# Performance work log

Measured on AMD Instinct MI355X. Metric: run time of the kernel, lower is better.

Reference implementation:

```python
import jax, jax.numpy as jnp
import numpy as np

DIM = 2048
N_HEADS = 16
KV_LORA = 512
NOPE = 128
ROPE = 64
V_DIM = 128
QK_DIM = NOPE + ROPE  # 192
B, S = 2, 2048
ROPE_THETA = 10000.0
ROPE_FACTOR = 40.0
BETA_FAST, BETA_SLOW = 32, 1
ORIG_LEN, MAX_LEN = 4096, 16384
MSCALE_ARG = 1.0
EPS = 1e-6


def _precompute_freqs(seqlen):
    # DeepSeek YaRN-corrected rotary frequencies (interleaved-pair convention).
    d = ROPE
    freqs = 1.0 / (ROPE_THETA ** (np.arange(0, d, 2, dtype=np.float64) / d))
    if MAX_LEN > ORIG_LEN:
        def corr_dim(n_rot):
            return d * np.log(ORIG_LEN / (n_rot * 2 * np.pi)) / (2 * np.log(ROPE_THETA))
        low = max(int(np.floor(corr_dim(BETA_FAST))), 0)
        high = min(int(np.ceil(corr_dim(BETA_SLOW))), d - 1)
        smooth = 1.0 - np.clip((np.arange(d // 2) - low) / max(high - low, 1e-3), 0, 1)
        freqs = freqs / ROPE_FACTOR * (1 - smooth) + freqs * smooth
    t = np.arange(seqlen, dtype=np.float64)
    ang = np.outer(t, freqs)  # [S, d/2]
    return np.cos(ang).astype(np.float32), np.sin(ang).astype(np.float32)


def softmax_scale():
    scale = QK_DIM ** -0.5
    if MAX_LEN > ORIG_LEN:
        m = 0.1 * MSCALE_ARG * float(np.log(ROPE_FACTOR)) + 1.0
        scale = scale * m * m
    return scale


def setup_inputs() -> dict:
    key = jax.random.key(0)
    ks = jax.random.split(key, 6)
    w_std = 0.02
    fc, fs = _precompute_freqs(S)
    return {
        "x": jax.random.normal(ks[0], (B, S, DIM), jnp.float32),
        "wq": jax.random.normal(ks[1], (N_HEADS * QK_DIM, DIM), jnp.float32) * w_std,
        "wkv_a": jax.random.normal(ks[2], (KV_LORA + ROPE, DIM), jnp.float32) * w_std,
        "kv_norm_w": jnp.ones((KV_LORA,), jnp.float32),
        "wkv_b": jax.random.normal(ks[3], (N_HEADS * (NOPE + V_DIM), KV_LORA), jnp.float32) * w_std,
        "wo": jax.random.normal(ks[4], (DIM, N_HEADS * V_DIM), jnp.float32) * w_std,
        "freqs_cos": jnp.asarray(fc),
        "freqs_sin": jnp.asarray(fs),
    }


def _apply_rotary(x, cos, sin):
    # x: [B, S, H, d]; interleaved complex pairs, cos/sin: [S, d/2]
    xr = x.reshape(*x.shape[:-1], -1, 2)
    x_re, x_im = xr[..., 0], xr[..., 1]
    c = cos[None, :, None, :]
    s = sin[None, :, None, :]
    y_re = x_re * c - x_im * s
    y_im = x_re * s + x_im * c
    return jnp.stack((y_re, y_im), axis=-1).reshape(x.shape)


def _rmsnorm(x, w):
    return x * jax.lax.rsqrt(jnp.mean(x * x, axis=-1, keepdims=True) + EPS) * w


def reference(x, wq, wkv_a, kv_norm_w, wkv_b, wo, freqs_cos, freqs_sin):
    b, s, _ = x.shape
    # Q projection (q_lora_rank == 0 path)
    q = (x @ wq.T).reshape(b, s, N_HEADS, QK_DIM)
    q_nope, q_pe = q[..., :NOPE], q[..., NOPE:]
    q_pe = _apply_rotary(q_pe, freqs_cos, freqs_sin)
    # Low-rank KV compression
    kv = x @ wkv_a.T  # [B, S, 512+64]
    kv_c, k_pe = kv[..., :KV_LORA], kv[..., KV_LORA:]
    k_pe = _apply_rotary(k_pe[:, :, None, :], freqs_cos, freqs_sin)  # [B,S,1,64]
    kv_c = _rmsnorm(kv_c, kv_norm_w)
    kvb = (kv_c @ wkv_b.T).reshape(b, s, N_HEADS, NOPE + V_DIM)
    k_nope, v = kvb[..., :NOPE], kvb[..., NOPE:]
    k = jnp.concatenate([k_nope, jnp.broadcast_to(k_pe, (b, s, N_HEADS, ROPE))], axis=-1)
    # Causal attention
    scores = jnp.einsum("bshd,bthd->bhst", q, k) * softmax_scale()
    causal = jnp.tril(jnp.ones((s, s), bool))
    scores = jnp.where(causal[None, None], scores, jnp.float32(-1e30))
    p = jax.nn.softmax(scores, axis=-1)
    out = jnp.einsum("bhst,bthd->bshd", p, v).reshape(b, s, N_HEADS * V_DIM)
    return out @ wo.T
```

## Files before the change

### kernel.cpp

```cpp
#include <hip/hip_runtime.h>
#include <math.h>

#define NH      16
#define D_NOPE  128
#define D_ROPE  64
#define D_QK    192
#define D_V     128
#define KV_LORA 512
#define NB      2
#define SEQ     2048
#define NTOK    (NB*SEQ)
#define QROW    (NH*D_QK)
#define KVBROW  (NH*(D_NOPE+D_V))
#define EPSF    1e-6f

typedef unsigned short u16;
typedef float  floatx4 __attribute__((ext_vector_type(4)));
typedef __bf16 bf16x8  __attribute__((ext_vector_type(8)));
typedef u16    u16x4   __attribute__((ext_vector_type(4)));
typedef u16    u16x8   __attribute__((ext_vector_type(8)));

__device__ __forceinline__ u16 f2bf(float f) {
    unsigned u = __builtin_bit_cast(unsigned, f);
    return (u16)((u + 0x7fffu + ((u >> 16) & 1u)) >> 16);
}

__device__ __forceinline__ void async_copy16(const void* g, void* l) {
    __builtin_amdgcn_global_load_lds(
        (const __attribute__((address_space(1))) unsigned int*)g,
        (__attribute__((address_space(3))) unsigned int*)l,
        16, 0, 0);
}

__global__ __launch_bounds__(256) void cast_all(const float* __restrict__ x,
                                                const float* __restrict__ wq,
                                                const float* __restrict__ wkva,
                                                const float* __restrict__ wkvb,
                                                const float* __restrict__ wo,
                                                u16* __restrict__ xb,
                                                u16* __restrict__ wqb,
                                                u16* __restrict__ wkvab,
                                                u16* __restrict__ wkvbb,
                                                u16* __restrict__ wob) {
    int blk = blockIdx.x;
    const float* src; u16* dst; bool pad = false;
    if (blk < 8192)        { src = x;    dst = xb; }
    else if (blk < 14336)  { blk -= 8192;  src = wq;   dst = wqb; }
    else if (blk < 15616)  { blk -= 14336; src = wkva; dst = wkvab; pad = true; }
    else if (blk < 17664)  { blk -= 15616; src = wkvb; dst = wkvbb; }
    else                   { blk -= 17664; src = wo;   dst = wob; }
    const int i = (blk * 256 + threadIdx.x) * 4;
    u16x4 o;
    if (pad && (i >> 11) >= 576) {
        o[0] = 0; o[1] = 0; o[2] = 0; o[3] = 0;
    } else {
        const float4 v = *(const float4*)&src[i];
        o[0] = f2bf(v.x); o[1] = f2bf(v.y); o[2] = f2bf(v.z); o[3] = f2bf(v.w);
    }
    *(u16x4*)&dst[i] = o;
}

template<int MODE>
__global__ __launch_bounds__(256) void gemm_mfma(const u16* __restrict__ A,
                                                 const u16* __restrict__ B,
                                                 void* __restrict__ Cout,
                                                 u16* __restrict__ kbuf,
                                                 u16* __restrict__ vT,
                                                 int M, int N, int K) {
    __shared__ u16 As[128 * 32];
    __shared__ u16 Bs[128 * 32];
    const int tid  = threadIdx.x;
    const int wave = tid >> 6, lane = tid & 63;
    const int m0 = blockIdx.y * 128, n0 = blockIdx.x * 128;
    const int wm = (wave & 1) * 64, wn = (wave >> 1) * 64;

    const int srow = wave * 32 + (lane >> 2);
    const int kch  = (lane & 3) * 8;
    const u16* gA0 = A + (size_t)(m0 + srow) * K + kch;
    const u16* gA1 = gA0 + (size_t)16 * K;
    const u16* gB0 = B + (size_t)(n0 + srow) * K + kch;
    const u16* gB1 = gB0 + (size_t)16 * K;
    u16* lA0 = &As[(wave * 32) * 32];
    u16* lA1 = &As[(wave * 32 + 16) * 32];
    u16* lB0 = &Bs[(wave * 32) * 32];
    u16* lB1 = &Bs[(wave * 32 + 16) * 32];

    floatx4 acc[4][4];
#pragma unroll
    for (int i = 0; i < 4; ++i)
#pragma unroll
        for (int j = 0; j < 4; ++j) acc[i][j] = 0.f;

    const int lrow = lane & 15;
    const int lkh  = (lane >> 4) * 8;

    for (int k0 = 0; k0 < K; k0 += 32) {
        __syncthreads();
        async_copy16(gA0 + k0, lA0);
        async_copy16(gA1 + k0, lA1);
        async_copy16(gB0 + k0, lB0);
        async_copy16(gB1 + k0, lB1);
        __syncthreads();
        bf16x8 a[4], b[4];
#pragma unroll
        for (int mi = 0; mi < 4; ++mi)
            a[mi] = *(const bf16x8*)&As[(wm + mi * 16 + lrow) * 32 + lkh];
#pragma unroll
        for (int ni = 0; ni < 4; ++ni)
            b[ni] = *(const bf16x8*)&Bs[(wn + ni * 16 + lrow) * 32 + lkh];
#pragma unroll
        for (int mi = 0; mi < 4; ++mi)
#pragma unroll
            for (int ni = 0; ni < 4; ++ni)
                acc[mi][ni] = __builtin_amdgcn_mfma_f32_16x16x32_bf16(
                    a[mi], b[ni], acc[mi][ni], 0, 0, 0);
    }

    const int crow = (lane >> 4) * 4, ccol = lane & 15;
#pragma unroll
    for (int mi = 0; mi < 4; ++mi)
#pragma unroll
        for (int ni = 0; ni < 4; ++ni) {
            const int m = m0 + wm + mi * 16 + crow;
            const int c = n0 + wn + ni * 16 + ccol;
            if (MODE == 0) {
                float* cp = (float*)Cout + (size_t)m * N + c;
#pragma unroll
                for (int r = 0; r < 4; ++r) cp[(size_t)r * N] = acc[mi][ni][r];
            } else if (MODE == 1) {
                u16* cp = (u16*)Cout + (size_t)m * N + c;
#pragma unroll
                for (int r = 0; r < 4; ++r) cp[(size_t)r * N] = f2bf(acc[mi][ni][r]);
            } else {
                const int hh = c >> 8, j = c & 255;
                const int bb = m >> 11, t = m & 2047;
                if (j < 128) {
#pragma unroll
                    for (int r = 0; r < 4; ++r)
                        kbuf[(((size_t)hh * 2 + bb) * 2048 + t + r) * 192 + j] =
                            f2bf(acc[mi][ni][r]);
                } else {
                    u16x4 pk;
#pragma unroll
                    for (int r = 0; r < 4; ++r) pk[r] = f2bf(acc[mi][ni][r]);
                    *(u16x4*)&vT[(((size_t)hh * 2 + bb) * 128 + (j - 128)) * 2048 + t] = pk;
                }
            }
        }
}


__global__ __launch_bounds__(256) void kv_fix(const float* __restrict__ kv_raw,
                                              const float* __restrict__ w,
                                              const float* __restrict__ fcos,
                                              const float* __restrict__ fsin,
                                              u16* __restrict__ kvn_bf,
                                              u16* __restrict__ kbuf) {
    const int row = blockIdx.x;
    const int tid = threadIdx.x;
    const float* src = kv_raw + (size_t)row * 640;
    const float v0 = src[tid];
    const float v1 = src[256 + tid];
    float ss = v0 * v0 + v1 * v1;
#pragma unroll
    for (int off = 32; off > 0; off >>= 1) ss += __shfl_down(ss, off, 64);
    __shared__ float red[4];
    __shared__ float kpe_s[64];
    if ((tid & 63) == 0) red[tid >> 6] = ss;
    if (tid < 32) {
        const int s = row & (SEQ - 1);
        const float c  = fcos[s * 32 + tid];
        const float sn = fsin[s * 32 + tid];
        const float xr = src[KV_LORA + 2 * tid];
        const float xi = src[KV_LORA + 2 * tid + 1];
        kpe_s[2 * tid]     = xr * c - xi * sn;
        kpe_s[2 * tid + 1] = xr * sn + xi * c;
    }
    __syncthreads();
    const float tot = red[0] + red[1] + red[2] + red[3];
    const float inv = rsqrtf(tot * (1.0f / KV_LORA) + EPSF);
    kvn_bf[(size_t)row * KV_LORA + tid]       = f2bf(v0 * inv * w[tid]);
    kvn_bf[(size_t)row * KV_LORA + 256 + tid] = f2bf(v1 * inv * w[256 + tid]);
    const int bb = row >> 11, t = row & 2047;
    const int hh = tid >> 4, dg = (tid & 15) * 4;
    u16x4 pk;
#pragma unroll
    for (int j = 0; j < 4; ++j) pk[j] = f2bf(kpe_s[dg + j]);
    *(u16x4*)&kbuf[(((size_t)hh * 2 + bb) * 2048 + t) * 192 + 128 + dg] = pk;
}

__global__ __launch_bounds__(256, 2) void attn_mfma(const u16* __restrict__ qbf,
                                                    const u16* __restrict__ kbuf,
                                                    const u16* __restrict__ vT,
                                                    u16* __restrict__ att,
                                                    float scale) {
    __shared__ __attribute__((aligned(16))) u16 Ks[2][6 * 64 * 32];
    __shared__ __attribute__((aligned(16))) u16 Vs[2 * 128 * 32];
    __shared__ __attribute__((aligned(16))) u16 Ps[4][16 * 72];
    const int x = blockIdx.x;
    const int qt_base = (x & 1) ? (15 - (x >> 1)) : (x >> 1);
    const int qt = blockIdx.z ? (15 - qt_base) : qt_base;
    const int h = blockIdx.y, b = blockIdx.z;
    const int tid = threadIdx.x, wave = tid >> 6, lane = tid & 63;
    const int l15 = lane & 15, lg = lane >> 4;
    const int lgs = lg ^ ((l15 >> 1) & 3);

    const u16* kb_base = kbuf + ((size_t)(h * 2 + b)) * 2048 * 192;
    const u16* vt_base = vT   + ((size_t)(h * 2 + b)) * 128 * 2048;

    int qrow[2];
    bf16x8 qf[2][6];
#pragma unroll
    for (int g = 0; g < 2; ++g) {
        qrow[g] = qt * 128 + g * 64 + wave * 16 + l15;
        const size_t qoff = ((size_t)(b * SEQ + qrow[g])) * QROW + h * 192 + lg * 8;
#pragma unroll
        for (int s = 0; s < 6; ++s) qf[g][s] = *(const bf16x8*)&qbf[qoff + s * 32];
    }

    floatx4 oacc[2][8];
#pragma unroll
    for (int g = 0; g < 2; ++g)
#pragma unroll
        for (int v = 0; v < 8; ++v) oacc[g][v] = 0.f;
    float m_run[2] = {-1e30f, -1e30f}, l_run[2] = {0.f, 0.f};

    auto stageK = [&](int bufi, int tt) {
#pragma unroll
        for (int i = 0; i < 6; ++i) {
            const int base = (wave * 6 + i) * 64;
            const int slot = base + lane;
            const int s = slot >> 8, r = slot & 255, tk = r >> 2, ch = r & 3;
            const int chs = ch ^ ((tk >> 1) & 3);
            async_copy16(kb_base + ((size_t)(tt + tk)) * 192 + s * 32 + chs * 8,
                         &Ks[bufi][base * 8]);
        }
    };
    auto stageV = [&](int tt) {
#pragma unroll
        for (int i = 0; i < 4; ++i) {
            const int base = (wave * 4 + i) * 64;
            const int slot = base + lane;
            const int s = slot >> 9, r = slot & 511, v = r >> 2, ch = r & 3;
            const int chs = ch ^ ((v >> 1) & 3);
            async_copy16(vt_base + ((size_t)v) * 2048 + tt + s * 32 + chs * 8,
                         &Vs[base * 8]);
        }
    };

    const int kt_max = 2 * qt + 1;
    stageK(0, 0);

    for (int kt = 0; kt <= kt_max; ++kt) {
        const int t0 = kt * 64;
        const int cur = kt & 1;

        stageV(t0);
        if (kt < kt_max) {
            stageK(cur ^ 1, t0 + 64);
            asm volatile("s_waitcnt vmcnt(10)" ::: "memory");
        } else {
            asm volatile("s_waitcnt vmcnt(4)" ::: "memory");
        }
        __builtin_amdgcn_s_barrier();

        floatx4 sacc[2][4];
#pragma unroll
        for (int g = 0; g < 2; ++g)
#pragma unroll
            for (int mt = 0; mt < 4; ++mt) sacc[g][mt] = 0.f;
        __builtin_amdgcn_s_setprio(1);
#pragma unroll
        for (int s = 0; s < 6; ++s) {
#pragma unroll
            for (int mt = 0; mt < 4; ++mt) {
                const bf16x8 kf = *(const bf16x8*)&Ks[cur][(s * 64 + mt * 16 + l15) * 32 + lgs * 8];
#pragma unroll
                for (int g = 0; g < 2; ++g)
                    sacc[g][mt] = __builtin_amdgcn_mfma_f32_16x16x32_bf16(
                        kf, qf[g][s], sacc[g][mt], 0, 0, 0);
            }
        }
        __builtin_amdgcn_s_setprio(0);

        u16x4 pk[2][4];
#pragma unroll
        for (int g = 0; g < 2; ++g) {
            const bool full = (t0 + 63) <= (qt * 128 + g * 64 + wave * 16);
            float p[16];
            float tmax = -1e30f;
#pragma unroll
            for (int mt = 0; mt < 4; ++mt)
#pragma unroll
                for (int r = 0; r < 4; ++r) {
                    float v = sacc[g][mt][r] * scale;
                    if (!full) {
                        const int tglob = t0 + mt * 16 + lg * 4 + r;
                        v = (tglob <= qrow[g]) ? v : -1e30f;
                    }
                    p[mt * 4 + r] = v;
                    tmax = fmaxf(tmax, v);
                }
            tmax = fmaxf(tmax, __shfl_xor(tmax, 16));
            tmax = fmaxf(tmax, __shfl_xor(tmax, 32));
            const bool defer = __all(tmax <= m_run[g] + 8.0f);
            float alph = 1.0f;
            float mnew = m_run[g];
            if (!defer) {
                mnew = fmaxf(m_run[g], tmax);
                alph = __expf(m_run[g] - mnew);
                m_run[g] = mnew;
            }
            float rsum = 0.f;
#pragma unroll
            for (int k = 0; k < 16; ++k) { p[k] = __expf(p[k] - mnew); rsum += p[k]; }
            rsum += __shfl_xor(rsum, 16);
            rsum += __shfl_xor(rsum, 32);
            if (!defer) {
                l_run[g] = l_run[g] * alph + rsum;
                float af[4];
#pragma unroll
                for (int r = 0; r < 4; ++r) af[r] = __shfl(alph, lg * 4 + r);
#pragma unroll
                for (int vt = 0; vt < 8; ++vt)
#pragma unroll
                    for (int r = 0; r < 4; ++r) oacc[g][vt][r] *= af[r];
            } else {
                l_run[g] += rsum;
            }
#pragma unroll
            for (int mt = 0; mt < 4; ++mt)
#pragma unroll
                for (int r = 0; r < 4; ++r) pk[g][mt][r] = f2bf(p[mt * 4 + r]);
        }

        bf16x8 pf[2][2];
#pragma unroll
        for (int g = 0; g < 2; ++g) {
#pragma unroll
            for (int mt = 0; mt < 4; ++mt)
                *(u16x4*)&Ps[wave][l15 * 72 + mt * 16 + lg * 4] = pk[g][mt];
#pragma unroll
            for (int s = 0; s < 2; ++s)
                pf[g][s] = *(const bf16x8*)&Ps[wave][l15 * 72 + s * 32 + lg * 8];
        }

        if (kt < kt_max) asm volatile("s_waitcnt vmcnt(6)" ::: "memory");
        else             asm volatile("s_waitcnt vmcnt(0)" ::: "memory");
        __builtin_amdgcn_s_barrier();

        __builtin_amdgcn_s_setprio(1);
#pragma unroll
        for (int s = 0; s < 2; ++s)
#pragma unroll
            for (int vt = 0; vt < 8; ++vt) {
                const bf16x8 vf = *(const bf16x8*)&Vs[(s * 128 + vt * 16 + l15) * 32 + lgs * 8];
                oacc[0][vt] = __builtin_amdgcn_mfma_f32_16x16x32_bf16(
                    pf[0][s], vf, oacc[0][vt], 0, 0, 0);
                oacc[1][vt] = __builtin_amdgcn_mfma_f32_16x16x32_bf16(
                    pf[1][s], vf, oacc[1][vt], 0, 0, 0);
            }
        __builtin_amdgcn_s_setprio(0);

        __builtin_amdgcn_s_barrier();
    }
#pragma unroll
    for (int g = 0; g < 2; ++g) {
        float lf[4];
#pragma unroll
        for (int r = 0; r < 4; ++r) lf[r] = 1.0f / __shfl(l_run[g], lg * 4 + r);
#pragma unroll
        for (int vt = 0; vt < 8; ++vt)
#pragma unroll
            for (int r = 0; r < 4; ++r) {
                const int orow = b * SEQ + qt * 128 + g * 64 + wave * 16 + lg * 4 + r;
                att[(size_t)orow * 2048 + h * 128 + vt * 16 + l15] =
                    f2bf(oacc[g][vt][r] * lf[r]);
            }
    }
}

extern "C" void kernel_launch(void* const* d_in, const int* in_sizes, int n_in,
                              void* d_out, int out_size, void* d_ws, size_t ws_size,
                              hipStream_t stream) {
    const float* x     = (const float*)d_in[0];
    const float* wq    = (const float*)d_in[1];
    const float* wkv_a = (const float*)d_in[2];
    const float* knw   = (const float*)d_in[3];
    const float* wkv_b = (const float*)d_in[4];
    const float* wo    = (const float*)d_in[5];
    const float* fcos  = (const float*)d_in[6];
    const float* fsin  = (const float*)d_in[7];
    float* out = (float*)d_out;

    char* w = (char*)d_ws;
    u16*   x_bf    = (u16*)w;  w += (size_t)NTOK * 2048 * 2;
    u16*   wq_bf   = (u16*)w;  w += (size_t)QROW * 2048 * 2;
    u16*   wkva_bf = (u16*)w;  w += (size_t)640 * 2048 * 2;
    u16*   wkvb_bf = (u16*)w;  w += (size_t)KVBROW * KV_LORA * 2;
    u16*   wo_bf   = (u16*)w;  w += (size_t)2048 * 2048 * 2;
    u16*   q_bf    = (u16*)w;  w += (size_t)NTOK * QROW * 2;
    float* kv_raw  = (float*)w; w += (size_t)NTOK * 640 * 4;
    u16*   kvn_bf  = (u16*)w;  w += (size_t)NTOK * KV_LORA * 2;
    u16*   kbuf    = (u16*)w;  w += (size_t)NH * NB * SEQ * 192 * 2;
    u16*   vT      = (u16*)w;  w += (size_t)NH * NB * 128 * SEQ * 2;
    u16*   att_bf  = (u16*)w;  w += (size_t)NTOK * 2048 * 2;

    const double mm = 0.1 * 1.0 * log(40.0) + 1.0;
    const float scale = (float)((1.0 / sqrt((double)D_QK)) * mm * mm);

    dim3 blk(256);
    cast_all<<<dim3(21760), blk, 0, stream>>>(x, wq, wkv_a, wkv_b, wo,
                                              x_bf, wq_bf, wkva_bf, wkvb_bf, wo_bf);
    gemm_mfma<1><<<dim3(QROW / 128, NTOK / 128), blk, 0, stream>>>(
        x_bf, wq_bf, q_bf, nullptr, nullptr, NTOK, QROW, 2048);
    gemm_mfma<0><<<dim3(640 / 128, NTOK / 128), blk, 0, stream>>>(
        x_bf, wkva_bf, kv_raw, nullptr, nullptr, NTOK, 640, 2048);
    kv_fix<<<dim3(NTOK), blk, 0, stream>>>(kv_raw, knw, fcos, fsin, kvn_bf, kbuf);
    gemm_mfma<2><<<dim3(KVBROW / 128, NTOK / 128), blk, 0, stream>>>(
        kvn_bf, wkvb_bf, nullptr, kbuf, vT, NTOK, KVBROW, KV_LORA);
    attn_mfma<<<dim3(SEQ / 128, NH, NB), blk, 0, stream>>>(q_bf, kbuf, vT, att_bf, scale);
    gemm_mfma<0><<<dim3(2048 / 128, NTOK / 128), blk, 0, stream>>>(
        att_bf, wo_bf, out, nullptr, nullptr, NTOK, 2048, 2048);
}
```

Baseline: 432.4 us.

## Balance causal attention work by pairing short and long query chunks per wave

Result: slower. 488.7 us (+13.0%).

```diff
diff --git a/kernel.cpp b/kernel.cpp
--- a/kernel.cpp
+++ b/kernel.cpp
@@ -197,25 +197,51 @@
     __shared__ __attribute__((aligned(16))) u16 Ks[2][6 * 64 * 32];
     __shared__ __attribute__((aligned(16))) u16 Vs[2 * 128 * 32];
     __shared__ __attribute__((aligned(16))) u16 Ps[4][16 * 72];
-    const int x = blockIdx.x;
-    const int qt_base = (x & 1) ? (15 - (x >> 1)) : (x >> 1);
-    const int qt = blockIdx.z ? (15 - qt_base) : qt_base;
+    const int j = blockIdx.x;
     const int h = blockIdx.y, b = blockIdx.z;
     const int tid = threadIdx.x, wave = tid >> 6, lane = tid & 63;
     const int l15 = lane & 15, lg = lane >> 4;
     const int lgs = lg ^ ((l15 >> 1) & 3);
 
+    const int c0 = j + 16 * wave;
+    const int c1 = j + 16 * (7 - wave);
+    const int ktmax0 = c0 >> 2;
+    const int ktmax1 = c1 >> 2;
+    const int KT = 28 + (j >> 2);
+
     const u16* kb_base = kbuf + ((size_t)(h * 2 + b)) * 2048 * 192;
     const u16* vt_base = vT   + ((size_t)(h * 2 + b)) * 128 * 2048;
 
-    int qrow[2];
+    const int qmin[2] = {16 * c0, 16 * c1};
+    const int qrow[2] = {16 * c0 + l15, 16 * c1 + l15};
     bf16x8 qf[2][6];
 #pragma unroll
     for (int g = 0; g < 2; ++g) {
-        qrow[g] = qt * 128 + g * 64 + wave * 16 + l15;
         const size_t qoff = ((size_t)(b * SEQ + qrow[g])) * QROW + h * 192 + lg * 8;
 #pragma unroll
         for (int s = 0; s < 6; ++s) qf[g][s] = *(const bf16x8*)&qbf[qoff + s * 32];
+    }
+
+    const u16* ksrc[6]; u16* kdstA[6]; u16* kdstB[6];
+#pragma unroll
+    for (int i = 0; i < 6; ++i) {
+        const int base = (wave * 6 + i) * 64;
+        const int slot = base + lane;
+        const int s = slot >> 8, r = slot & 255, tk = r >> 2, ch = r & 3;
+        const int chs = ch ^ ((tk >> 1) & 3);
+        ksrc[i]  = kb_base + (size_t)tk * 192 + s * 32 + chs * 8;
+        kdstA[i] = &Ks[0][base * 8];
+        kdstB[i] = &Ks[1][base * 8];
+    }
+    const u16* vsrc[4]; u16* vdst[4];
+#pragma unroll
+    for (int i = 0; i < 4; ++i) {
+        const int base = (wave * 4 + i) * 64;
+        const int slot = base + lane;
+        const int s = slot >> 9, r = slot & 511, v = r >> 2, ch = r & 3;
+        const int chs = ch ^ ((v >> 1) & 3);
+        vsrc[i] = vt_base + (size_t)v * 2048 + s * 32 + chs * 8;
+        vdst[i] = &Vs[base * 8];
     }
 
     floatx4 oacc[2][8];
@@ -225,39 +251,21 @@
         for (int v = 0; v < 8; ++v) oacc[g][v] = 0.f;
     float m_run[2] = {-1e30f, -1e30f}, l_run[2] = {0.f, 0.f};
 
-    auto stageK = [&](int bufi, int tt) {
-#pragma unroll
-        for (int i = 0; i < 6; ++i) {
-            const int base = (wave * 6 + i) * 64;
-            const int slot = base + lane;
-            const int s = slot >> 8, r = slot & 255, tk = r >> 2, ch = r & 3;
-            const int chs = ch ^ ((tk >> 1) & 3);
-            async_copy16(kb_base + ((size_t)(tt + tk)) * 192 + s * 32 + chs * 8,
-                         &Ks[bufi][base * 8]);
-        }
-    };
-    auto stageV = [&](int tt) {
-#pragma unroll
-        for (int i = 0; i < 4; ++i) {
-            const int base = (wave * 4 + i) * 64;
-            const int slot = base + lane;
-            const int s = slot >> 9, r = slot & 511, v = r >> 2, ch = r & 3;
-            const int chs = ch ^ ((v >> 1) & 3);
-            async_copy16(vt_base + ((size_t)v) * 2048 + tt + s * 32 + chs * 8,
-                         &Vs[base * 8]);
-        }
-    };
-
-    const int kt_max = 2 * qt + 1;
-    stageK(0, 0);
-
-    for (int kt = 0; kt <= kt_max; ++kt) {
+#pragma unroll
+    for (int i = 0; i < 6; ++i) async_copy16(ksrc[i], kdstA[i]);
+
+    for (int kt = 0; kt <= KT; ++kt) {
         const int t0 = kt * 64;
         const int cur = kt & 1;
-
-        stageV(t0);
-        if (kt < kt_max) {
-            stageK(cur ^ 1, t0 + 64);
+        const bool act0 = (kt <= ktmax0), act1 = (kt <= ktmax1);
+
+#pragma unroll
+        for (int i = 0; i < 4; ++i) async_copy16(vsrc[i] + t0, vdst[i]);
+        if (kt < KT) {
+            const size_t koff = (size_t)(t0 + 64) * 192;
+            u16* const* kd = cur ? kdstA : kdstB;
+#pragma unroll
+            for (int i = 0; i < 6; ++i) async_copy16(ksrc[i] + koff, kd[i]);
             asm volatile("s_waitcnt vmcnt(10)" ::: "memory");
         } else {
             asm volatile("s_waitcnt vmcnt(4)" ::: "memory");
@@ -269,24 +277,37 @@
         for (int g = 0; g < 2; ++g)
 #pragma unroll
             for (int mt = 0; mt < 4; ++mt) sacc[g][mt] = 0.f;
-        __builtin_amdgcn_s_setprio(1);
-#pragma unroll
-        for (int s = 0; s < 6; ++s) {
-#pragma unroll
-            for (int mt = 0; mt < 4; ++mt) {
-                const bf16x8 kf = *(const bf16x8*)&Ks[cur][(s * 64 + mt * 16 + l15) * 32 + lgs * 8];
-#pragma unroll
-                for (int g = 0; g < 2; ++g)
-                    sacc[g][mt] = __builtin_amdgcn_mfma_f32_16x16x32_bf16(
-                        kf, qf[g][s], sacc[g][mt], 0, 0, 0);
-            }
-        }
-        __builtin_amdgcn_s_setprio(0);
+        if (act1) {
+            __builtin_amdgcn_s_setprio(1);
+            if (act0) {
+#pragma unroll
+                for (int s = 0; s < 6; ++s)
+#pragma unroll
+                    for (int mt = 0; mt < 4; ++mt) {
+                        const bf16x8 kf = *(const bf16x8*)&Ks[cur][(s * 64 + mt * 16 + l15) * 32 + lgs * 8];
+                        sacc[0][mt] = __builtin_amdgcn_mfma_f32_16x16x32_bf16(
+                            kf, qf[0][s], sacc[0][mt], 0, 0, 0);
+                        sacc[1][mt] = __builtin_amdgcn_mfma_f32_16x16x32_bf16(
+                            kf, qf[1][s], sacc[1][mt], 0, 0, 0);
+                    }
+            } else {
+#pragma unroll
+                for (int s = 0; s < 6; ++s)
+#pragma unroll
+                    for (int mt = 0; mt < 4; ++mt) {
+                        const bf16x8 kf = *(const bf16x8*)&Ks[cur][(s * 64 + mt * 16 + l15) * 32 + lgs * 8];
+                        sacc[1][mt] = __builtin_amdgcn_mfma_f32_16x16x32_bf16(
+                            kf, qf[1][s], sacc[1][mt], 0, 0, 0);
+                    }
+            }
+            __builtin_amdgcn_s_setprio(0);
+        }
 
         u16x4 pk[2][4];
 #pragma unroll
         for (int g = 0; g < 2; ++g) {
-            const bool full = (t0 + 63) <= (qt * 128 + g * 64 + wave * 16);
+            if (!(g ? act1 : act0)) continue;
+            const bool full = (t0 + 63) <= qmin[g];
             float p[16];
             float tmax = -1e30f;
 #pragma unroll
@@ -337,6 +358,7 @@
         bf16x8 pf[2][2];
 #pragma unroll
         for (int g = 0; g < 2; ++g) {
+            if (!(g ? act1 : act0)) continue;
 #pragma unroll
             for (int mt = 0; mt < 4; ++mt)
                 *(u16x4*)&Ps[wave][l15 * 72 + mt * 16 + lg * 4] = pk[g][mt];
@@ -345,22 +367,35 @@
                 pf[g][s] = *(const bf16x8*)&Ps[wave][l15 * 72 + s * 32 + lg * 8];
         }
 
-        if (kt < kt_max) asm volatile("s_waitcnt vmcnt(6)" ::: "memory");
-        else             asm volatile("s_waitcnt vmcnt(0)" ::: "memory");
+        if (kt < KT) asm volatile("s_waitcnt vmcnt(6)" ::: "memory");
+        else         asm volatile("s_waitcnt vmcnt(0)" ::: "memory");
         __builtin_amdgcn_s_barrier();
 
-        __builtin_amdgcn_s_setprio(1);
-#pragma unroll
-        for (int s = 0; s < 2; ++s)
-#pragma unroll
-            for (int vt = 0; vt < 8; ++vt) {
-                const bf16x8 vf = *(const bf16x8*)&Vs[(s * 128 + vt * 16 + l15) * 32 + lgs * 8];
-                oacc[0][vt] = __builtin_amdgcn_mfma_f32_16x16x32_bf16(
-                    pf[0][s], vf, oacc[0][vt], 0, 0, 0);
-                oacc[1][vt] = __builtin_amdgcn_mfma_f32_16x16x32_bf16(
-                    pf[1][s], vf, oacc[1][vt], 0, 0, 0);
-            }
-        __builtin_amdgcn_s_setprio(0);
+        if (act1) {
+            __builtin_amdgcn_s_setprio(1);
+            if (act0) {
+#pragma unroll
+                for (int s = 0; s < 2; ++s)
+#pragma unroll
+                    for (int vt = 0; vt < 8; ++vt) {
+                        const bf16x8 vf = *(const bf16x8*)&Vs[(s * 128 + vt * 16 + l15) * 32 + lgs * 8];
+                        oacc[0][vt] = __builtin_amdgcn_mfma_f32_16x16x32_bf16(
+                            pf[0][s], vf, oacc[0][vt], 0, 0, 0);
+                        oacc[1][vt] = __builtin_amdgcn_mfma_f32_16x16x32_bf16(
+                            pf[1][s], vf, oacc[1][vt], 0, 0, 0);
+                    }
+            } else {
+#pragma unroll
+                for (int s = 0; s < 2; ++s)
+#pragma unroll
+                    for (int vt = 0; vt < 8; ++vt) {
+                        const bf16x8 vf = *(const bf16x8*)&Vs[(s * 128 + vt * 16 + l15) * 32 + lgs * 8];
+                        oacc[1][vt] = __builtin_amdgcn_mfma_f32_16x16x32_bf16(
+                            pf[1][s], vf, oacc[1][vt], 0, 0, 0);
+                    }
+            }
+            __builtin_amdgcn_s_setprio(0);
+        }
 
         __builtin_amdgcn_s_barrier();
     }
@@ -373,7 +408,7 @@
         for (int vt = 0; vt < 8; ++vt)
 #pragma unroll
             for (int r = 0; r < 4; ++r) {
-                const int orow = b * SEQ + qt * 128 + g * 64 + wave * 16 + lg * 4 + r;
+                const int orow = b * SEQ + qmin[g] + lg * 4 + r;
                 att[(size_t)orow * 2048 + h * 128 + vt * 16 + l15] =
                     f2bf(oacc[g][vt][r] * lf[r]);
             }
@@ -419,7 +454,7 @@
     kv_fix<<<dim3(NTOK), blk, 0, stream>>>(kv_raw, knw, fcos, fsin, kvn_bf, kbuf);
     gemm_mfma<2><<<dim3(KVBROW / 128, NTOK / 128), blk, 0, stream>>>(
         kvn_bf, wkvb_bf, nullptr, kbuf, vT, NTOK, KVBROW, KV_LORA);
-    attn_mfma<<<dim3(SEQ / 128, NH, NB), blk, 0, stream>>>(q_bf, kbuf, vT, att_bf, scale);
+    attn_mfma<<<dim3(16, NH, NB), blk, 0, stream>>>(q_bf, kbuf, vT, att_bf, scale);
     gemm_mfma<0><<<dim3(2048 / 128, NTOK / 128), blk, 0, stream>>>(
         att_bf, wo_bf, out, nullptr, nullptr, NTOK, 2048, 2048);
 }
```

## Pair complementary causal q-tiles per 8-wave block with shared double-buffered K/V

Applied to the files above, without the earlier changes.

New measurement: 468.0 us. 8.2% more time.

```diff
diff --git a/kernel.cpp b/kernel.cpp
--- a/kernel.cpp
+++ b/kernel.cpp
@@ -189,18 +189,20 @@
     *(u16x4*)&kbuf[(((size_t)hh * 2 + bb) * 2048 + t) * 192 + 128 + dg] = pk;
 }
 
-__global__ __launch_bounds__(256, 2) void attn_mfma(const u16* __restrict__ qbf,
+#define KS_HALF (6 * 64 * 32)
+#define VS_HALF (2 * 128 * 32)
+__global__ __launch_bounds__(512, 2) void attn_mfma(const u16* __restrict__ qbf,
                                                     const u16* __restrict__ kbuf,
                                                     const u16* __restrict__ vT,
                                                     u16* __restrict__ att,
                                                     float scale) {
-    __shared__ __attribute__((aligned(16))) u16 Ks[2][6 * 64 * 32];
-    __shared__ __attribute__((aligned(16))) u16 Vs[2 * 128 * 32];
-    __shared__ __attribute__((aligned(16))) u16 Ps[4][16 * 72];
-    const int x = blockIdx.x;
-    const int qt_base = (x & 1) ? (15 - (x >> 1)) : (x >> 1);
-    const int qt = blockIdx.z ? (15 - qt_base) : qt_base;
-    const int h = blockIdx.y, b = blockIdx.z;
+    __shared__ __attribute__((aligned(16))) u16 KsF[2 * KS_HALF];
+    __shared__ __attribute__((aligned(16))) u16 VsF[2 * VS_HALF];
+    __shared__ __attribute__((aligned(16))) u16 Ps[8][16 * 72];
+    const int hb = blockIdx.x;
+    const int qa = blockIdx.y;
+    const int qb = 15 - qa;
+    const int h = hb >> 1, b = hb & 1;
     const int tid = threadIdx.x, wave = tid >> 6, lane = tid & 63;
     const int l15 = lane & 15, lg = lane >> 4;
     const int lgs = lg ^ ((l15 >> 1) & 3);
@@ -208,14 +210,41 @@
     const u16* kb_base = kbuf + ((size_t)(h * 2 + b)) * 2048 * 192;
     const u16* vt_base = vT   + ((size_t)(h * 2 + b)) * 128 * 2048;
 
-    int qrow[2];
+    const int qbase0 = qa * 128 + wave * 16;
+    const int qbase1 = qb * 128 + wave * 16;
     bf16x8 qf[2][6];
-#pragma unroll
-    for (int g = 0; g < 2; ++g) {
-        qrow[g] = qt * 128 + g * 64 + wave * 16 + l15;
-        const size_t qoff = ((size_t)(b * SEQ + qrow[g])) * QROW + h * 192 + lg * 8;
-#pragma unroll
-        for (int s = 0; s < 6; ++s) qf[g][s] = *(const bf16x8*)&qbf[qoff + s * 32];
+    {
+        const size_t q0 = ((size_t)(b * SEQ + qbase0 + l15)) * QROW + h * 192 + lg * 8;
+        const size_t q1 = ((size_t)(b * SEQ + qbase1 + l15)) * QROW + h * 192 + lg * 8;
+#pragma unroll
+        for (int s = 0; s < 6; ++s) {
+            qf[0][s] = *(const bf16x8*)&qbf[q0 + s * 32];
+            qf[1][s] = *(const bf16x8*)&qbf[q1 + s * 32];
+        }
+    }
+
+    const u16* ksrc0; const u16* ksrc1; const u16* ksrc2;
+    int kbo0, kbo1, kbo2;
+    {
+        const int b0 = (wave * 3 + 0) * 64, s0 = (b0 + lane) >> 8, r0 = (b0 + lane) & 255;
+        const int b1 = (wave * 3 + 1) * 64, s1 = (b1 + lane) >> 8, r1 = (b1 + lane) & 255;
+        const int b2 = (wave * 3 + 2) * 64, s2 = (b2 + lane) >> 8, r2 = (b2 + lane) & 255;
+        const int tk0 = r0 >> 2, tk1 = r1 >> 2, tk2 = r2 >> 2;
+        ksrc0 = kb_base + (size_t)tk0 * 192 + s0 * 32 + ((r0 & 3) ^ ((tk0 >> 1) & 3)) * 8;
+        ksrc1 = kb_base + (size_t)tk1 * 192 + s1 * 32 + ((r1 & 3) ^ ((tk1 >> 1) & 3)) * 8;
+        ksrc2 = kb_base + (size_t)tk2 * 192 + s2 * 32 + ((r2 & 3) ^ ((tk2 >> 1) & 3)) * 8;
+        kbo0 = b0 * 8; kbo1 = b1 * 8; kbo2 = b2 * 8;
+    }
+    const u16* vsrc0; const u16* vsrc1;
+    int vbo0, vbo1;
+    {
+        const int b0 = (wave * 2 + 0) * 64, s0 = (b0 + lane) >> 9, r0 = (b0 + lane) & 511;
+        const int b1 = (wave * 2 + 1) * 64, s1 = (b1 + lane) >> 9, r1 = (b1 + lane) & 511;
+        const int v0 = r0 >> 2, v1 = r1 >> 2;
+        vsrc0 = vt_base + (size_t)v0 * 2048 + s0 * 32 + ((r0 & 3) ^ ((v0 >> 1) & 3)) * 8;
+        vsrc1 = vt_base + (size_t)v1 * 2048 + s1 * 32 + ((v1 >> 1 & 3) != 0 ? ((r1 & 3) ^ ((v1 >> 1) & 3)) : (r1 & 3)) * 8;
+        vsrc1 = vt_base + (size_t)v1 * 2048 + s1 * 32 + ((r1 & 3) ^ ((v1 >> 1) & 3)) * 8;
+        vbo0 = b0 * 8; vbo1 = b1 * 8;
     }
 
     floatx4 oacc[2][8];
@@ -225,78 +254,80 @@
         for (int v = 0; v < 8; ++v) oacc[g][v] = 0.f;
     float m_run[2] = {-1e30f, -1e30f}, l_run[2] = {0.f, 0.f};
 
-    auto stageK = [&](int bufi, int tt) {
-#pragma unroll
-        for (int i = 0; i < 6; ++i) {
-            const int base = (wave * 6 + i) * 64;
-            const int slot = base + lane;
-            const int s = slot >> 8, r = slot & 255, tk = r >> 2, ch = r & 3;
-            const int chs = ch ^ ((tk >> 1) & 3);
-            async_copy16(kb_base + ((size_t)(tt + tk)) * 192 + s * 32 + chs * 8,
-                         &Ks[bufi][base * 8]);
-        }
-    };
-    auto stageV = [&](int tt) {
-#pragma unroll
-        for (int i = 0; i < 4; ++i) {
-            const int base = (wave * 4 + i) * 64;
-            const int slot = base + lane;
-            const int s = slot >> 9, r = slot & 511, v = r >> 2, ch = r & 3;
-            const int chs = ch ^ ((v >> 1) & 3);
-            async_copy16(vt_base + ((size_t)v) * 2048 + tt + s * 32 + chs * 8,
-                         &Vs[base * 8]);
-        }
-    };
-
-    const int kt_max = 2 * qt + 1;
-    stageK(0, 0);
-
-    for (int kt = 0; kt <= kt_max; ++kt) {
+    const int nt = 32 - 2 * qa;
+    const int ktmax0 = 2 * qa + 1;
+
+    async_copy16(ksrc0, &KsF[kbo0]);
+    async_copy16(ksrc1, &KsF[kbo1]);
+    async_copy16(ksrc2, &KsF[kbo2]);
+    async_copy16(vsrc0, &VsF[vbo0]);
+    async_copy16(vsrc1, &VsF[vbo1]);
+
+    for (int kt = 0; kt < nt; ++kt) {
         const int t0 = kt * 64;
         const int cur = kt & 1;
-
-        stageV(t0);
-        if (kt < kt_max) {
-            stageK(cur ^ 1, t0 + 64);
-            asm volatile("s_waitcnt vmcnt(10)" ::: "memory");
+        const int kco = cur * KS_HALF;
+        const int vco = cur * VS_HALF;
+        const bool act0 = (kt <= ktmax0);
+
+        asm volatile("s_waitcnt vmcnt(0)" ::: "memory");
+        __builtin_amdgcn_s_barrier();
+
+        if (kt + 1 < nt) {
+            const int kno = (cur ^ 1) * KS_HALF;
+            const int vno = (cur ^ 1) * VS_HALF;
+            const size_t ko = (size_t)(t0 + 64) * 192;
+            async_copy16(ksrc0 + ko, &KsF[kno + kbo0]);
+            async_copy16(ksrc1 + ko, &KsF[kno + kbo1]);
+            async_copy16(ksrc2 + ko, &KsF[kno + kbo2]);
+            async_copy16(vsrc0 + t0 + 64, &VsF[vno + vbo0]);
+            async_copy16(vsrc1 + t0 + 64, &VsF[vno + vbo1]);
+        }
+
+        floatx4 sacc0[4], sacc1[4];
+#pragma unroll
+        for (int mt = 0; mt < 4; ++mt) { sacc0[mt] = 0.f; sacc1[mt] = 0.f; }
+        __builtin_amdgcn_s_setprio(1);
+        if (act0) {
+#pragma unroll
+            for (int s = 0; s < 6; ++s)
+#pragma unroll
+                for (int mt = 0; mt < 4; ++mt) {
+                    const bf16x8 kf = *(const bf16x8*)&KsF[kco + (s * 64 + mt * 16 + l15) * 32 + lgs * 8];
+                    sacc0[mt] = __builtin_amdgcn_mfma_f32_16x16x32_bf16(
+                        kf, qf[0][s], sacc0[mt], 0, 0, 0);
+                    sacc1[mt] = __builtin_amdgcn_mfma_f32_16x16x32_bf16(
+                        kf, qf[1][s], sacc1[mt], 0, 0, 0);
+                }
         } else {
-            asm volatile("s_waitcnt vmcnt(4)" ::: "memory");
-        }
-        __builtin_amdgcn_s_barrier();
-
-        floatx4 sacc[2][4];
-#pragma unroll
-        for (int g = 0; g < 2; ++g)
-#pragma unroll
-            for (int mt = 0; mt < 4; ++mt) sacc[g][mt] = 0.f;
-        __builtin_amdgcn_s_setprio(1);
-#pragma unroll
-        for (int s = 0; s < 6; ++s) {
-#pragma unroll
-            for (int mt = 0; mt < 4; ++mt) {
-                const bf16x8 kf = *(const bf16x8*)&Ks[cur][(s * 64 + mt * 16 + l15) * 32 + lgs * 8];
-#pragma unroll
-                for (int g = 0; g < 2; ++g)
-                    sacc[g][mt] = __builtin_amdgcn_mfma_f32_16x16x32_bf16(
-                        kf, qf[g][s], sacc[g][mt], 0, 0, 0);
-            }
+#pragma unroll
+            for (int s = 0; s < 6; ++s)
+#pragma unroll
+                for (int mt = 0; mt < 4; ++mt) {
+                    const bf16x8 kf = *(const bf16x8*)&KsF[kco + (s * 64 + mt * 16 + l15) * 32 + lgs * 8];
+                    sacc1[mt] = __builtin_amdgcn_mfma_f32_16x16x32_bf16(
+                        kf, qf[1][s], sacc1[mt], 0, 0, 0);
+                }
         }
         __builtin_amdgcn_s_setprio(0);
 
-        u16x4 pk[2][4];
+        bf16x8 pf[2][2];
 #pragma unroll
         for (int g = 0; g < 2; ++g) {
-            const bool full = (t0 + 63) <= (qt * 128 + g * 64 + wave * 16);
+            if (g == 0 && !act0) continue;
+            floatx4* sc = g ? sacc1 : sacc0;
+            const int qbase = g ? qbase1 : qbase0;
+            const bool full = (t0 + 63) <= qbase;
             float p[16];
             float tmax = -1e30f;
 #pragma unroll
             for (int mt = 0; mt < 4; ++mt)
 #pragma unroll
                 for (int r = 0; r < 4; ++r) {
-                    float v = sacc[g][mt][r] * scale;
+                    float v = sc[mt][r] * scale;
                     if (!full) {
                         const int tglob = t0 + mt * 16 + lg * 4 + r;
-                        v = (tglob <= qrow[g]) ? v : -1e30f;
+                        v = (tglob <= qbase + l15) ? v : -1e30f;
                     }
                     p[mt * 4 + r] = v;
                     tmax = fmaxf(tmax, v);
@@ -304,68 +335,66 @@
             tmax = fmaxf(tmax, __shfl_xor(tmax, 16));
             tmax = fmaxf(tmax, __shfl_xor(tmax, 32));
             const bool defer = __all(tmax <= m_run[g] + 8.0f);
-            float alph = 1.0f;
             float mnew = m_run[g];
             if (!defer) {
                 mnew = fmaxf(m_run[g], tmax);
-                alph = __expf(m_run[g] - mnew);
+                const float alph = __expf(m_run[g] - mnew);
                 m_run[g] = mnew;
+                float af[4];
+#pragma unroll
+                for (int r = 0; r < 4; ++r) af[r] = __shfl(alph, lg * 4 + r);
+#pragma unroll
+                for (int vt = 0; vt < 8; ++vt)
+#pragma unroll
+                    for (int r = 0; r < 4; ++r) oacc[g][vt][r] *= af[r];
+                l_run[g] *= alph;
             }
             float rsum = 0.f;
 #pragma unroll
             for (int k = 0; k < 16; ++k) { p[k] = __expf(p[k] - mnew); rsum += p[k]; }
             rsum += __shfl_xor(rsum, 16);
             rsum += __shfl_xor(rsum, 32);
-            if (!defer) {
-                l_run[g] = l_run[g] * alph + rsum;
-                float af[4];
-#pragma unroll
-                for (int r = 0; r < 4; ++r) af[r] = __shfl(alph, lg * 4 + r);
-#pragma unroll
-                for (int vt = 0; vt < 8; ++vt)
-#pragma unroll
-                    for (int r = 0; r < 4; ++r) oacc[g][vt][r] *= af[r];
-            } else {
-                l_run[g] += rsum;
+            l_run[g] += rsum;
+#pragma unroll
+            for (int mt = 0; mt < 4; ++mt) {
+                u16x4 pk;
+#pragma unroll
+                for (int r = 0; r < 4; ++r) pk[r] = f2bf(p[mt * 4 + r]);
+                *(u16x4*)&Ps[wave][l15 * 72 + mt * 16 + lg * 4] = pk;
             }
-#pragma unroll
-            for (int mt = 0; mt < 4; ++mt)
-#pragma unroll
-                for (int r = 0; r < 4; ++r) pk[g][mt][r] = f2bf(p[mt * 4 + r]);
-        }
-
-        bf16x8 pf[2][2];
-#pragma unroll
-        for (int g = 0; g < 2; ++g) {
-#pragma unroll
-            for (int mt = 0; mt < 4; ++mt)
-                *(u16x4*)&Ps[wave][l15 * 72 + mt * 16 + lg * 4] = pk[g][mt];
 #pragma unroll
             for (int s = 0; s < 2; ++s)
                 pf[g][s] = *(const bf16x8*)&Ps[wave][l15 * 72 + s * 32 + lg * 8];
         }
 
-        if (kt < kt_max) asm volatile("s_waitcnt vmcnt(6)" ::: "memory");
-        else             asm volatile("s_waitcnt vmcnt(0)" ::: "memory");
-        __builtin_amdgcn_s_barrier();
-
         __builtin_amdgcn_s_setprio(1);
-#pragma unroll
-        for (int s = 0; s < 2; ++s)
-#pragma unroll
-            for (int vt = 0; vt < 8; ++vt) {
-                const bf16x8 vf = *(const bf16x8*)&Vs[(s * 128 + vt * 16 + l15) * 32 + lgs * 8];
-                oacc[0][vt] = __builtin_amdgcn_mfma_f32_16x16x32_bf16(
-                    pf[0][s], vf, oacc[0][vt], 0, 0, 0);
-                oacc[1][vt] = __builtin_amdgcn_mfma_f32_16x16x32_bf16(
-                    pf[1][s], vf, oacc[1][vt], 0, 0, 0);
-            }
+        if (act0) {
+#pragma unroll
+            for (int s = 0; s < 2; ++s)
+#pragma unroll
+                for (int vt = 0; vt < 8; ++vt) {
+                    const bf16x8 vf = *(const bf16x8*)&VsF[vco + (s * 128 + vt * 16 + l15) * 32 + lgs * 8];
+                    oacc[0][vt] = __builtin_amdgcn_mfma_f32_16x16x32_bf16(
+                        pf[0][s], vf, oacc[0][vt], 0, 0, 0);
+                    oacc[1][vt] = __builtin_amdgcn_mfma_f32_16x16x32_bf16(
+                        pf[1][s], vf, oacc[1][vt], 0, 0, 0);
+                }
+        } else {
+#pragma unroll
+            for (int s = 0; s < 2; ++s)
+#pragma unroll
+                for (int vt = 0; vt < 8; ++vt) {
+                    const bf16x8 vf = *(const bf16x8*)&VsF[vco + (s * 128 + vt * 16 + l15) * 32 + lgs * 8];
+                    oacc[1][vt] = __builtin_amdgcn_mfma_f32_16x16x32_bf16(
+                        pf[1][s], vf, oacc[1][vt], 0, 0, 0);
+                }
+        }
         __builtin_amdgcn_s_setprio(0);
-
-        __builtin_amdgcn_s_barrier();
-    }
+    }
+
 #pragma unroll
     for (int g = 0; g < 2; ++g) {
+        const int qbase = g ? qbase1 : qbase0;
         float lf[4];
 #pragma unroll
         for (int r = 0; r < 4; ++r) lf[r] = 1.0f / __shfl(l_run[g], lg * 4 + r);
@@ -373,7 +402,7 @@
         for (int vt = 0; vt < 8; ++vt)
 #pragma unroll
             for (int r = 0; r < 4; ++r) {
-                const int orow = b * SEQ + qt * 128 + g * 64 + wave * 16 + lg * 4 + r;
+                const int orow = b * SEQ + qbase + lg * 4 + r;
                 att[(size_t)orow * 2048 + h * 128 + vt * 16 + l15] =
                     f2bf(oacc[g][vt][r] * lf[r]);
             }
@@ -419,7 +448,7 @@
     kv_fix<<<dim3(NTOK), blk, 0, stream>>>(kv_raw, knw, fcos, fsin, kvn_bf, kbuf);
     gemm_mfma<2><<<dim3(KVBROW / 128, NTOK / 128), blk, 0, stream>>>(
         kvn_bf, wkvb_bf, nullptr, kbuf, vT, NTOK, KVBROW, KV_LORA);
-    attn_mfma<<<dim3(SEQ / 128, NH, NB), blk, 0, stream>>>(q_bf, kbuf, vT, att_bf, scale);
+    attn_mfma<<<dim3(32, 8, 1), dim3(512), 0, stream>>>(q_bf, kbuf, vT, att_bf, scale);
     gemm_mfma<0><<<dim3(2048 / 128, NTOK / 128), blk, 0, stream>>>(
         att_bf, wo_bf, out, nullptr, nullptr, NTOK, 2048, 2048);
 }
```
